# Kernel optimization log

Measured on AMD Instinct MI355X. Metric: run time of the kernel, lower is better.

Reference implementation:

```python
import jax, jax.numpy as jnp
import numpy as np

B, C, H, W = 8, 64, 256, 256
M1, M2 = 16, 16  # half of n_modes=(32,32); rfft last dim keeps n_modes[-1]//2


def setup_inputs() -> dict:
    key = jax.random.key(0)
    ks = jax.random.split(key, 7)
    scale = 1.0 / (C * C)
    return {
        "x": jax.random.normal(ks[0], (B, C, H, W), dtype=jnp.float32),
        "w1r": scale * jax.random.normal(ks[1], (C, C, M1, M2), dtype=jnp.float32),
        "w1i": scale * jax.random.normal(ks[2], (C, C, M1, M2), dtype=jnp.float32),
        "w2r": scale * jax.random.normal(ks[3], (C, C, M1, M2), dtype=jnp.float32),
        "w2i": scale * jax.random.normal(ks[4], (C, C, M1, M2), dtype=jnp.float32),
        "conv_w": jax.random.normal(ks[5], (C, C), dtype=jnp.float32) / np.sqrt(C),
        "conv_b": jax.random.normal(ks[6], (C,), dtype=jnp.float32) * 0.01,
    }


def reference(x, w1r, w1i, w2r, w2i, conv_w, conv_b):
    # ---- SpectralConv branch ----
    # rfft2 over spatial dims with 'ortho' norm: [b, c, H, W//2+1] complex
    x_ft = jnp.fft.rfftn(x, axes=(2, 3), norm="ortho")
    w1 = w1r + 1j * w1i  # positive-frequency corner weights [i, o, m1, m2]
    w2 = w2r + 1j * w2i  # negative-frequency corner weights
    top = jnp.einsum("bixy,ioxy->boxy", x_ft[:, :, :M1, :M2], w1)
    bot = jnp.einsum("bixy,ioxy->boxy", x_ft[:, :, -M1:, :M2], w2)
    out_ft = jnp.zeros((B, C, H, W // 2 + 1), dtype=x_ft.dtype)
    out_ft = out_ft.at[:, :, :M1, :M2].set(top)
    out_ft = out_ft.at[:, :, -M1:, :M2].set(bot)
    x1 = jnp.fft.irfftn(out_ft, s=(H, W), axes=(2, 3), norm="ortho")
    # ---- 1x1 Conv1d residual branch (channel mixing) ----
    x2 = jnp.einsum("oi,bixy->boxy", conv_w, x) + conv_b[None, :, None, None]
    return x1 + x2
```

## Files before the change

kernel.cpp:

```cpp
#include <hip/hip_runtime.h>
#include <math.h>


#define TWOPI_256 0.024543692606170259f
#define INV256    0.00390625f

#define NX   262144
#define NWT  2097152
#define NZ   2097152
#define O_TA  0
#define O_TB  4096
#define O_XR  20480
#define O_XI  (O_XR + NX)
#define O_WTR (O_XI + NX)
#define O_WTI (O_WTR + NWT)
#define O_YRA (O_WTI + NWT)
#define O_YIA (O_YRA + NX)
#define O_ZR  (O_YIA + NX)
#define O_ZI  (O_ZR + NZ)
#define O_TT  (O_ZI + NZ)
#define O_TD  (O_TT + 4096)
#define O_YRB (O_TD + 16384)
#define O_YIB (O_YRB + NX)

using s16x8 = __attribute__((ext_vector_type(8))) short;
using f32x4 = __attribute__((ext_vector_type(4))) float;
using u32x4 = __attribute__((ext_vector_type(4))) unsigned;

__device__ __forceinline__ unsigned short f2bf(float f) {
    union { float f; unsigned u; } a; a.f = f;
    unsigned r = (a.u + 0x7fffu + ((a.u >> 16) & 1u)) >> 16;
    return (unsigned short)r;
}

__device__ __forceinline__ unsigned bfpack(float a, float b) {
    union { float f; unsigned u; } x, y; x.f = a; y.f = b;
    return ((x.u + 0x8000u) >> 16) | ((y.u + 0x8000u) & 0xffff0000u);
}

__global__ __launch_bounds__(256) void ktabs(unsigned short* __restrict__ tA,
                                             unsigned short* __restrict__ tB,
                                             unsigned short* __restrict__ tD,
                                             unsigned short* __restrict__ tT) {
    int idx = blockIdx.x * 256 + threadIdx.x;
    if (idx < 8192) {
        int col = idx >> 8, w = idx & 255;
        int ky = col & 15;
        int mm = (ky * w) & 255;
        float s, c; sincosf((float)mm * TWOPI_256, &s, &c);
        tA[idx] = f2bf(col < 16 ? c * INV256 : -s * INV256);
    } else if (idx < 40960) {
        int j = idx - 8192;
        int kx2 = j >> 9, k = j & 511, h = k >> 1, p = k & 1;
        int kxi = kx2 & 31;
        int kx = (kxi < 16) ? kxi : (224 + kxi);
        int mm = (kx * h) & 255;
        float s, c; sincosf((float)mm * TWOPI_256, &s, &c);
        float v;
        if (kx2 < 32) v = p ? s : c;
        else          v = p ? c : -s;
        tB[j] = f2bf(v);
    } else if (idx < 73728) {
        int j = idx - 40960;
        int ri = j >> 14, rem = j & 16383;
        int h = rem >> 6, k = rem & 63, kxi = k >> 1, p = k & 1;
        int kx = (kxi < 16) ? kxi : (224 + kxi);
        int mm = (kx * h) & 255;
        float s, c; sincosf((float)mm * TWOPI_256, &s, &c);
        float v;
        if (ri == 0) v = p ? -s : c;
        else         v = p ? c : s;
        tD[j] = f2bf(v);
    } else {
        int j = idx - 73728;
        int w = j >> 5, kk = j & 31, ky = kk >> 1;
        int mm = (ky * w) & 255;
        float s, c; sincosf((float)mm * TWOPI_256, &s, &c);
        tT[j] = f2bf((kk & 1) ? -s : c);
    }
}

__global__ __launch_bounds__(256, 2) void kab_fwd(const float* __restrict__ x,
                                                  const unsigned short* __restrict__ tA,
                                                  const unsigned short* __restrict__ tB,
                                                  float* __restrict__ Xr,
                                                  float* __restrict__ Xi) {
    __shared__ __align__(16) unsigned short xt[16384];
    __shared__ __align__(16) unsigned int   ub[4096];
    const int tid  = threadIdx.x;
    const int bc   = blockIdx.x;
    const int m    = tid & 15;
    const int g    = (tid >> 4) & 3;
    const int wave = tid >> 6;

    const float* xp = x + (size_t)bc * 65536;
    const int hh = tid >> 4;
    const int w4 = tid & 15;

    f32x4 acc[2][4];
#pragma unroll
    for (int a = 0; a < 2; ++a)
#pragma unroll
        for (int fn = 0; fn < 4; ++fn)
#pragma unroll
            for (int r = 0; r < 4; ++r) acc[a][fn][r] = 0.f;

    float4 stg[2][16];
#pragma unroll
    for (int it = 0; it < 16; ++it)
        stg[0][it] = *reinterpret_cast<const float4*>(xp + (it * 16 + hh) * 256 + w4 * 4);

#pragma unroll
    for (int ch = 0; ch < 4; ++ch) {
        const int cur = ch & 1;
        if (ch < 3) {
#pragma unroll
            for (int it = 0; it < 16; ++it)
                stg[cur ^ 1][it] = *reinterpret_cast<const float4*>(
                    xp + (it * 16 + hh) * 256 + (ch + 1) * 64 + w4 * 4);
        }
#pragma unroll
        for (int it = 0; it < 16; ++it) {
            int h = it * 16 + hh;
            float4 v = stg[cur][it];
            unsigned lo = bfpack(v.x, v.y);
            unsigned hi = bfpack(v.z, v.w);
            int wl  = w4 * 4;
            int blk = (wl >> 3) ^ (h & 7);
            char* p = reinterpret_cast<char*>(xt) + (h << 7) + (blk << 4) + ((wl & 7) << 1);
            *reinterpret_cast<uint2*>(p) = make_uint2(lo, hi);
        }
        __syncthreads();
#pragma unroll
        for (int ks = 0; ks < 2; ++ks) {
            s16x8 a0 = *reinterpret_cast<const s16x8*>(tA + m * 256        + ch * 64 + ks * 32 + 8 * g);
            s16x8 a1 = *reinterpret_cast<const s16x8*>(tA + (16 + m) * 256 + ch * 64 + ks * 32 + 8 * g);
#pragma unroll
            for (int fn = 0; fn < 4; ++fn) {
                int h   = wave * 64 + fn * 16 + m;
                int blk = (4 * ks + g) ^ (h & 7);
                s16x8 bf = *reinterpret_cast<const s16x8*>(
                    reinterpret_cast<const char*>(xt) + (h << 7) + (blk << 4));
                acc[0][fn] = __builtin_amdgcn_mfma_f32_16x16x32_bf16(a0, bf, acc[0][fn], 0, 0, 0);
                acc[1][fn] = __builtin_amdgcn_mfma_f32_16x16x32_bf16(a1, bf, acc[1][fn], 0, 0, 0);
            }
        }
        __syncthreads();
    }

#pragma unroll
    for (int fn = 0; fn < 4; ++fn) {
        int h = wave * 64 + fn * 16 + m;
#pragma unroll
        for (int r = 0; r < 4; ++r) {
            int ky = 4 * g + r;
            unsigned pk = bfpack(acc[0][fn][r], acc[1][fn][r]);
            int blk = (h >> 2) ^ (ky & 7);
            ub[ky * 256 + blk * 4 + (h & 3)] = pk;
        }
    }
    __syncthreads();

    f32x4 acc2;
#pragma unroll
    for (int r = 0; r < 4; ++r) acc2[r] = 0.f;
#pragma unroll
    for (int ks = 0; ks < 16; ++ks) {
        s16x8 a2 = *reinterpret_cast<const s16x8*>(tB + (wave * 16 + m) * 512 + ks * 32 + 8 * g);
        int blk = (4 * ks + g) ^ (m & 7);
        s16x8 b2 = *reinterpret_cast<const s16x8*>(
            reinterpret_cast<const char*>(ub) + m * 1024 + (blk << 4));
        acc2 = __builtin_amdgcn_mfma_f32_16x16x32_bf16(a2, b2, acc2, 0, 0, 0);
    }
#pragma unroll
    for (int r = 0; r < 4; ++r) {
        int kx2 = wave * 16 + 4 * g + r;
        if (kx2 < 32) Xr[(size_t)bc * 512 + kx2 * 16 + m]        = acc2[r];
        else          Xi[(size_t)bc * 512 + (kx2 - 32) * 16 + m] = acc2[r];
    }
}

__global__ __launch_bounds__(256) void kw_prep(const float* __restrict__ w1r,
                                               const float* __restrict__ w1i,
                                               const float* __restrict__ w2r,
                                               const float* __restrict__ w2i,
                                               float* __restrict__ Wtr,
                                               float* __restrict__ Wti) {
    __shared__ float lds[128][65];
    const int tid = threadIdx.x;
    const int a = blockIdx.x >> 6;
    const int i = blockIdx.x & 63;
    const float* src = (a == 0) ? w1r : (a == 1) ? w1i : (a == 2) ? w2r : w2i;
    float* dst = (a & 1) ? Wti : Wtr;
    const int kxoff = (a >> 1) << 4;
    const float* sp = src + (size_t)i * 16384;

    for (int p = 0; p < 2; ++p) {
        if (p) __syncthreads();
#pragma unroll
        for (int it = 0; it < 8; ++it) {
            int f4 = it * 256 + tid;
            int o = f4 >> 5, j4 = f4 & 31;
            float4 v = *reinterpret_cast<const float4*>(sp + o * 256 + p * 128 + j4 * 4);
            lds[j4 * 4 + 0][o] = v.x; lds[j4 * 4 + 1][o] = v.y;
            lds[j4 * 4 + 2][o] = v.z; lds[j4 * 4 + 3][o] = v.w;
        }
        __syncthreads();
        const int o = tid & 63, mq = tid >> 6;
#pragma unroll
        for (int r = 0; r < 32; ++r) {
            int lm = r * 4 + mq;
            int mky = p * 128 + lm;
            int mm = mky >> 4, ky = mky & 15;
            dst[((((size_t)(kxoff + mm)) * 16 + ky) * 64 + i) * 64 + o] = lds[lm][o];
        }
    }
}

__global__ __launch_bounds__(256) void kc_mix(const float* __restrict__ Xr,
                                              const float* __restrict__ Xi,
                                              const float* __restrict__ Wtr,
                                              const float* __restrict__ Wti,
                                              float* __restrict__ YrA,
                                              float* __restrict__ YiA,
                                              float* __restrict__ YrB,
                                              float* __restrict__ YiB) {
    __shared__ float xsr[256], xsi[256];
    const int tid  = threadIdx.x;
    const int mode = blockIdx.x >> 1;
    const int ih   = blockIdx.x & 1;
    {
        int b = tid >> 5, il = tid & 31;
        xsr[tid] = Xr[(size_t)(b * 64 + ih * 32 + il) * 512 + mode];
        xsi[tid] = Xi[(size_t)(b * 64 + ih * 32 + il) * 512 + mode];
    }
    __syncthreads();
    const int o = tid & 63, bg = tid >> 6;
    float yr0 = 0.f, yi0 = 0.f, yr1 = 0.f, yi1 = 0.f;
    const float* wrp = Wtr + (size_t)mode * 4096 + ih * 2048;
    const float* wip = Wti + (size_t)mode * 4096 + ih * 2048;
#pragma unroll 8
    for (int i = 0; i < 32; ++i) {
        float wr = wrp[i * 64 + o], wi = wip[i * 64 + o];
        float xr = xsr[bg * 32 + i],        xi = xsi[bg * 32 + i];
        yr0 += xr * wr - xi * wi;  yi0 += xr * wi + xi * wr;
        float xr2 = xsr[(bg + 4) * 32 + i], xi2 = xsi[(bg + 4) * 32 + i];
        yr1 += xr2 * wr - xi2 * wi;  yi1 += xr2 * wi + xi2 * wr;
    }
    float* Yr = ih ? YrB : YrA;
    float* Yi = ih ? YiB : YiA;
    const int kxi = mode >> 4, kym = mode & 15;
    const size_t e0 = ((size_t)bg * 64 + o) * 512 + kym * 32 + kxi;
    const size_t e1 = ((size_t)(bg + 4) * 64 + o) * 512 + kym * 32 + kxi;
    Yr[e0] = yr0;  Yi[e0] = yi0;
    Yr[e1] = yr1;  Yi[e1] = yi1;
}

__global__ __launch_bounds__(256) void kd_mfma(const float* __restrict__ YrA,
                                               const float* __restrict__ YiA,
                                               const float* __restrict__ YrB,
                                               const float* __restrict__ YiB,
                                               const unsigned short* __restrict__ tD,
                                               float* __restrict__ Zr,
                                               float* __restrict__ Zi) {
    __shared__ __align__(16) unsigned short at[4096];
    __shared__ __align__(16) float zt[64][68];
    const int tid = threadIdx.x;
    const int bid = blockIdx.x;
    const int b  = bid >> 7;
    const int og = (bid >> 3) & 15;
    const int ri = (bid >> 2) & 1;
    const int hs = bid & 3;

    {
        const int row = tid >> 2, q = tid & 3;
        const int ol = row >> 4, ky = row & 15;
        const float sc = (ky == 0) ? INV256 : 2.f * INV256;
        const size_t yb = ((size_t)(b * 64 + og * 4 + ol)) * 512 + ky * 32 + q * 8;
        f32x4 r0 = *reinterpret_cast<const f32x4*>(YrA + yb)     + *reinterpret_cast<const f32x4*>(YrB + yb);
        f32x4 r1 = *reinterpret_cast<const f32x4*>(YrA + yb + 4) + *reinterpret_cast<const f32x4*>(YrB + yb + 4);
        f32x4 i0 = *reinterpret_cast<const f32x4*>(YiA + yb)     + *reinterpret_cast<const f32x4*>(YiB + yb);
        f32x4 i1 = *reinterpret_cast<const f32x4*>(YiA + yb + 4) + *reinterpret_cast<const f32x4*>(YiB + yb + 4);
        unsigned wbuf[8];
#pragma unroll
        for (int t = 0; t < 4; ++t) {
            wbuf[t]     = bfpack(r0[t] * sc, i0[t] * sc);
            wbuf[4 + t] = bfpack(r1[t] * sc, i1[t] * sc);
        }
        char* base = reinterpret_cast<char*>(at) + row * 128;
        *reinterpret_cast<uint4*>(base + (((2 * q)     ^ (row & 7)) << 4)) = *reinterpret_cast<uint4*>(&wbuf[0]);
        *reinterpret_cast<uint4*>(base + (((2 * q + 1) ^ (row & 7)) << 4)) = *reinterpret_cast<uint4*>(&wbuf[4]);
    }
    __syncthreads();

    const int m = tid & 15, g = (tid >> 4) & 3, wid = tid >> 6;
    const unsigned short* td = tD + ri * 16384;
    const int hg = hs * 64 + wid * 16 + m;

    f32x4 acc[4];
#pragma unroll
    for (int mf = 0; mf < 4; ++mf)
#pragma unroll
        for (int r = 0; r < 4; ++r) acc[mf][r] = 0.f;

#pragma unroll
    for (int ks = 0; ks < 2; ++ks) {
        s16x8 bf = *reinterpret_cast<const s16x8*>(td + hg * 64 + ks * 32 + 8 * g);
#pragma unroll
        for (int mf = 0; mf < 4; ++mf) {
            s16x8 af = *reinterpret_cast<const s16x8*>(
                reinterpret_cast<const char*>(at) + (mf * 16 + m) * 128
                + (((4 * ks + g) ^ (m & 7)) << 4));
            acc[mf] = __builtin_amdgcn_mfma_f32_16x16x32_bf16(af, bf, acc[mf], 0, 0, 0);
        }
    }

#pragma unroll
    for (int mf = 0; mf < 4; ++mf)
#pragma unroll
        for (int r = 0; r < 4; ++r)
            zt[wid * 16 + m][mf * 16 + 4 * g + r] = acc[mf][r];
    __syncthreads();

    float* Zd = ri ? Zi : Zr;
    const int ol = tid >> 6, hloc = (tid >> 2) & 15, kg = tid & 3;
#pragma unroll
    for (int hq = 0; hq < 4; ++hq) {
        f32x4 v = *reinterpret_cast<const f32x4*>(&zt[hq * 16 + hloc][ol * 16 + 4 * kg]);
        size_t off = (((size_t)(b * 64 + og * 4 + ol)) * 256 + hs * 64 + hq * 16 + hloc) * 16 + 4 * kg;
        *reinterpret_cast<f32x4*>(Zd + off) = v;
    }
}

__global__ __launch_bounds__(256) void ke_mfma(const float* __restrict__ x,
                                               const float* __restrict__ Zr,
                                               const float* __restrict__ Zi,
                                               const float* __restrict__ cw,
                                               const float* __restrict__ bias,
                                               const unsigned short* __restrict__ ttab,
                                               float* __restrict__ out) {
    __shared__ unsigned int bsx[4096];
    const int tid = threadIdx.x;
    const int b  = blockIdx.x >> 9;
    const int h  = (blockIdx.x >> 1) & 255;
    const int wh = blockIdx.x & 1;
    const int wbase = wh * 128;

    const size_t xbase = ((size_t)b * 64) * 65536 + (size_t)h * 256 + wbase;
    const int wl4 = (tid & 31) * 4;
    const int ipg = tid >> 5;
    float4 va[4], vb[4];
#pragma unroll
    for (int it = 0; it < 4; ++it) {
        int ip = it * 8 + ipg;
        va[it] = *reinterpret_cast<const float4*>(x + xbase + (size_t)(2 * ip) * 65536 + wl4);
        vb[it] = *reinterpret_cast<const float4*>(x + xbase + (size_t)(2 * ip + 1) * 65536 + wl4);
    }

    const int m = tid & 15;
    const int g = (tid >> 4) & 3;
    const int wave = tid >> 6;
    const int o = wave * 16 + m;

    s16x8 a0, a1, az;
    {
        f32x4 p  = *reinterpret_cast<const f32x4*>(cw + o * 64 + 8 * g);
        f32x4 q  = *reinterpret_cast<const f32x4*>(cw + o * 64 + 8 * g + 4);
        f32x4 p2 = *reinterpret_cast<const f32x4*>(cw + o * 64 + 32 + 8 * g);
        f32x4 q2 = *reinterpret_cast<const f32x4*>(cw + o * 64 + 32 + 8 * g + 4);
        size_t zoff = (((size_t)b * 64 + o) * 256 + h) * 16 + 4 * g;
        f32x4 zr = *reinterpret_cast<const f32x4*>(Zr + zoff);
        f32x4 zi = *reinterpret_cast<const f32x4*>(Zi + zoff);
        u32x4 t0 = {bfpack(p[0], p[1]),  bfpack(p[2], p[3]),
                    bfpack(q[0], q[1]),  bfpack(q[2], q[3])};
        u32x4 t1 = {bfpack(p2[0], p2[1]), bfpack(p2[2], p2[3]),
                    bfpack(q2[0], q2[1]), bfpack(q2[2], q2[3])};
        u32x4 tz = {bfpack(zr[0], zi[0]), bfpack(zr[1], zi[1]),
                    bfpack(zr[2], zi[2]), bfpack(zr[3], zi[3])};
        a0 = __builtin_bit_cast(s16x8, t0);
        a1 = __builtin_bit_cast(s16x8, t1);
        az = __builtin_bit_cast(s16x8, tz);
    }
    s16x8 btr[8];
#pragma unroll
    for (int f = 0; f < 8; ++f) {
        int w = wbase + f * 16 + m;
        btr[f] = *reinterpret_cast<const s16x8*>(ttab + w * 32 + 8 * g);
    }
    f32x4 bv = *reinterpret_cast<const f32x4*>(bias + wave * 16 + 4 * g);

#pragma unroll
    for (int it = 0; it < 4; ++it) {
        int ip = it * 8 + ipg;
        const float* pa = reinterpret_cast<const float*>(&va[it]);
        const float* pb = reinterpret_cast<const float*>(&vb[it]);
#pragma unroll
        for (int j = 0; j < 4; ++j) {
            int wl = wl4 + j;
            int c = (wl ^ (wl >> 3)) & 7;
            unsigned pk = bfpack(pa[j], pb[j]);
            bsx[(wl << 5) + ((((ip >> 2) ^ c) << 2) | (ip & 3))] = pk;
        }
    }
    __syncthreads();

    f32x4 acc[8];
#pragma unroll
    for (int f = 0; f < 8; ++f)
#pragma unroll
        for (int r = 0; r < 4; ++r) acc[f][r] = 0.f;

#pragma unroll
    for (int f = 0; f < 8; ++f) {
        int wl = f * 16 + m;
        int c = (wl ^ (wl >> 3)) & 7;
        const char* rb = reinterpret_cast<const char*>(bsx) + (wl << 7);
        s16x8 bx0 = *reinterpret_cast<const s16x8*>(rb + ((g ^ c) << 4));
        s16x8 bx1 = *reinterpret_cast<const s16x8*>(rb + (((4 + g) ^ c) << 4));
        acc[f] = __builtin_amdgcn_mfma_f32_16x16x32_bf16(a0, bx0, acc[f], 0, 0, 0);
        acc[f] = __builtin_amdgcn_mfma_f32_16x16x32_bf16(a1, bx1, acc[f], 0, 0, 0);
        acc[f] = __builtin_amdgcn_mfma_f32_16x16x32_bf16(az, btr[f], acc[f], 0, 0, 0);
    }

    float* ob = out + ((size_t)(b * 64 + wave * 16 + 4 * g)) * 65536 + (size_t)h * 256 + wbase;
#pragma unroll
    for (int f = 0; f < 8; ++f) {
#pragma unroll
        for (int r = 0; r < 4; ++r)
            ob[(size_t)r * 65536 + f * 16 + m] = acc[f][r] + bv[r];
    }
}

extern "C" void kernel_launch(void* const* d_in, const int* in_sizes, int n_in,
                              void* d_out, int out_size, void* d_ws, size_t ws_size,
                              hipStream_t stream) {
    const float* x   = (const float*)d_in[0];
    const float* w1r = (const float*)d_in[1];
    const float* w1i = (const float*)d_in[2];
    const float* w2r = (const float*)d_in[3];
    const float* w2i = (const float*)d_in[4];
    const float* cw  = (const float*)d_in[5];
    const float* cb  = (const float*)d_in[6];
    float* out = (float*)d_out;
    float* ws  = (float*)d_ws;
    unsigned short* tA   = (unsigned short*)(ws + O_TA);
    unsigned short* tB   = (unsigned short*)(ws + O_TB);
    unsigned short* ttab = (unsigned short*)(ws + O_TT);
    unsigned short* tD   = (unsigned short*)(ws + O_TD);

    ktabs<<<320, 256, 0, stream>>>(tA, tB, tD, ttab);
    kw_prep<<<256, 256, 0, stream>>>(w1r, w1i, w2r, w2i, ws + O_WTR, ws + O_WTI);
    kab_fwd<<<512, 256, 0, stream>>>(x, tA, tB, ws + O_XR, ws + O_XI);
    kc_mix<<<1024, 256, 0, stream>>>(ws + O_XR, ws + O_XI, ws + O_WTR, ws + O_WTI,
                                     ws + O_YRA, ws + O_YIA, ws + O_YRB, ws + O_YIB);
    kd_mfma<<<1024, 256, 0, stream>>>(ws + O_YRA, ws + O_YIA, ws + O_YRB, ws + O_YIB,
                                      tD, ws + O_ZR, ws + O_ZI);
    ke_mfma<<<4096, 256, 0, stream>>>(x, ws + O_ZR, ws + O_ZI, cw, cb, ttab, out);
}
```

Before: 127.5 us.

## Split forward DFT over H halves and store Z intermediate as bf16

The forward-transform kernel now runs two blocks per (b,c) slice, each taking half of the H rows. Each half writes a partial spectrum to its own buffer, and the mixing kernel adds the two partials when it loads them. This halves LDS and register use per block, allowing occupancy 4 and twice as many blocks. Separately, the Z intermediate is written as packed bf16 in the layout the final kernel loads directly as an MFMA operand, which halves that traffic and removes the repacking. The cost is an extra partial buffer to read and sum, and the twiddle table layout changes to match.

```diff
diff --git a/kernel.cpp b/kernel.cpp
--- a/kernel.cpp
+++ b/kernel.cpp
@@ -7,21 +7,23 @@
 
 #define NX   262144
 #define NWT  2097152
-#define NZ   2097152
-#define O_TA  0
-#define O_TB  4096
-#define O_XR  20480
-#define O_XI  (O_XR + NX)
-#define O_WTR (O_XI + NX)
-#define O_WTI (O_WTR + NWT)
-#define O_YRA (O_WTI + NWT)
-#define O_YIA (O_YRA + NX)
-#define O_ZR  (O_YIA + NX)
-#define O_ZI  (O_ZR + NZ)
-#define O_TT  (O_ZI + NZ)
-#define O_TD  (O_TT + 4096)
-#define O_YRB (O_TD + 16384)
-#define O_YIB (O_YRB + NX)
+#define NZH  1048576
+#define O_TA   0
+#define O_TB   4096
+#define O_XRA  20480
+#define O_XIA  (O_XRA + NX)
+#define O_XRB  (O_XIA + NX)
+#define O_XIB  (O_XRB + NX)
+#define O_WTR  (O_XIB + NX)
+#define O_WTI  (O_WTR + NWT)
+#define O_YRA  (O_WTI + NWT)
+#define O_YIA  (O_YRA + NX)
+#define O_YRB  (O_YIA + NX)
+#define O_YIB  (O_YRB + NX)
+#define O_ZRB  (O_YIB + NX)
+#define O_ZIB  (O_ZRB + NZH)
+#define O_TT   (O_ZIB + NZH)
+#define O_TD   (O_TT + 4096)
 
 using s16x8 = __attribute__((ext_vector_type(8))) short;
 using f32x4 = __attribute__((ext_vector_type(4))) float;
@@ -73,41 +75,45 @@
         tD[j] = f2bf(v);
     } else {
         int j = idx - 73728;
-        int w = j >> 5, kk = j & 31, ky = kk >> 1;
+        int w = j >> 5, kk = j & 31, ky = kk & 15;
         int mm = (ky * w) & 255;
         float s, c; sincosf((float)mm * TWOPI_256, &s, &c);
-        tT[j] = f2bf((kk & 1) ? -s : c);
-    }
-}
-
-__global__ __launch_bounds__(256, 2) void kab_fwd(const float* __restrict__ x,
+        tT[j] = f2bf(kk < 16 ? c : -s);
+    }
+}
+
+__global__ __launch_bounds__(256, 4) void kab_fwd(const float* __restrict__ x,
                                                   const unsigned short* __restrict__ tA,
                                                   const unsigned short* __restrict__ tB,
-                                                  float* __restrict__ Xr,
-                                                  float* __restrict__ Xi) {
-    __shared__ __align__(16) unsigned short xt[16384];
-    __shared__ __align__(16) unsigned int   ub[4096];
+                                                  float* __restrict__ XrA,
+                                                  float* __restrict__ XiA,
+                                                  float* __restrict__ XrB,
+                                                  float* __restrict__ XiB) {
+    __shared__ __align__(16) unsigned short xt[8192];
+    __shared__ __align__(16) unsigned int   ub[2048];
     const int tid  = threadIdx.x;
-    const int bc   = blockIdx.x;
+    const int bc   = blockIdx.x >> 1;
+    const int hhf  = blockIdx.x & 1;
+    const int hbase = hhf << 7;
     const int m    = tid & 15;
     const int g    = (tid >> 4) & 3;
     const int wave = tid >> 6;
 
-    const float* xp = x + (size_t)bc * 65536;
+    const float* xp = x + (size_t)bc * 65536 + (size_t)hbase * 256;
     const int hh = tid >> 4;
     const int w4 = tid & 15;
 
-    f32x4 acc[2][4];
+    f32x4 acc[2][2];
 #pragma unroll
     for (int a = 0; a < 2; ++a)
 #pragma unroll
-        for (int fn = 0; fn < 4; ++fn)
+        for (int fn = 0; fn < 2; ++fn)
 #pragma unroll
             for (int r = 0; r < 4; ++r) acc[a][fn][r] = 0.f;
 
-    float4 stg[2][16];
-#pragma unroll
-    for (int it = 0; it < 16; ++it)
+    float4 stg[2][8];
+#pragma unroll
+    for (int it = 0; it < 8; ++it)
         stg[0][it] = *reinterpret_cast<const float4*>(xp + (it * 16 + hh) * 256 + w4 * 4);
 
 #pragma unroll
@@ -115,12 +121,12 @@
         const int cur = ch & 1;
         if (ch < 3) {
 #pragma unroll
-            for (int it = 0; it < 16; ++it)
+            for (int it = 0; it < 8; ++it)
                 stg[cur ^ 1][it] = *reinterpret_cast<const float4*>(
                     xp + (it * 16 + hh) * 256 + (ch + 1) * 64 + w4 * 4);
         }
 #pragma unroll
-        for (int it = 0; it < 16; ++it) {
+        for (int it = 0; it < 8; ++it) {
             int h = it * 16 + hh;
             float4 v = stg[cur][it];
             unsigned lo = bfpack(v.x, v.y);
@@ -136,8 +142,8 @@
             s16x8 a0 = *reinterpret_cast<const s16x8*>(tA + m * 256        + ch * 64 + ks * 32 + 8 * g);
             s16x8 a1 = *reinterpret_cast<const s16x8*>(tA + (16 + m) * 256 + ch * 64 + ks * 32 + 8 * g);
 #pragma unroll
-            for (int fn = 0; fn < 4; ++fn) {
-                int h   = wave * 64 + fn * 16 + m;
+            for (int fn = 0; fn < 2; ++fn) {
+                int h   = wave * 32 + fn * 16 + m;
                 int blk = (4 * ks + g) ^ (h & 7);
                 s16x8 bf = *reinterpret_cast<const s16x8*>(
                     reinterpret_cast<const char*>(xt) + (h << 7) + (blk << 4));
@@ -149,14 +155,14 @@
     }
 
 #pragma unroll
-    for (int fn = 0; fn < 4; ++fn) {
-        int h = wave * 64 + fn * 16 + m;
+    for (int fn = 0; fn < 2; ++fn) {
+        int h = wave * 32 + fn * 16 + m;
 #pragma unroll
         for (int r = 0; r < 4; ++r) {
             int ky = 4 * g + r;
             unsigned pk = bfpack(acc[0][fn][r], acc[1][fn][r]);
             int blk = (h >> 2) ^ (ky & 7);
-            ub[ky * 256 + blk * 4 + (h & 3)] = pk;
+            ub[ky * 128 + blk * 4 + (h & 3)] = pk;
         }
     }
     __syncthreads();
@@ -165,13 +171,15 @@
 #pragma unroll
     for (int r = 0; r < 4; ++r) acc2[r] = 0.f;
 #pragma unroll
-    for (int ks = 0; ks < 16; ++ks) {
-        s16x8 a2 = *reinterpret_cast<const s16x8*>(tB + (wave * 16 + m) * 512 + ks * 32 + 8 * g);
+    for (int ks = 0; ks < 8; ++ks) {
+        s16x8 a2 = *reinterpret_cast<const s16x8*>(tB + (wave * 16 + m) * 512 + hbase * 2 + ks * 32 + 8 * g);
         int blk = (4 * ks + g) ^ (m & 7);
         s16x8 b2 = *reinterpret_cast<const s16x8*>(
-            reinterpret_cast<const char*>(ub) + m * 1024 + (blk << 4));
+            reinterpret_cast<const char*>(ub) + m * 512 + (blk << 4));
         acc2 = __builtin_amdgcn_mfma_f32_16x16x32_bf16(a2, b2, acc2, 0, 0, 0);
     }
+    float* Xr = hhf ? XrB : XrA;
+    float* Xi = hhf ? XiB : XiA;
 #pragma unroll
     for (int r = 0; r < 4; ++r) {
         int kx2 = wave * 16 + 4 * g + r;
@@ -217,8 +225,10 @@
     }
 }
 
-__global__ __launch_bounds__(256) void kc_mix(const float* __restrict__ Xr,
-                                              const float* __restrict__ Xi,
+__global__ __launch_bounds__(256) void kc_mix(const float* __restrict__ XrA,
+                                              const float* __restrict__ XiA,
+                                              const float* __restrict__ XrB,
+                                              const float* __restrict__ XiB,
                                               const float* __restrict__ Wtr,
                                               const float* __restrict__ Wti,
                                               float* __restrict__ YrA,
@@ -231,8 +241,9 @@
     const int ih   = blockIdx.x & 1;
     {
         int b = tid >> 5, il = tid & 31;
-        xsr[tid] = Xr[(size_t)(b * 64 + ih * 32 + il) * 512 + mode];
-        xsi[tid] = Xi[(size_t)(b * 64 + ih * 32 + il) * 512 + mode];
+        size_t ofs = (size_t)(b * 64 + ih * 32 + il) * 512 + mode;
+        xsr[tid] = XrA[ofs] + XrB[ofs];
+        xsi[tid] = XiA[ofs] + XiB[ofs];
     }
     __syncthreads();
     const int o = tid & 63, bg = tid >> 6;
@@ -261,8 +272,8 @@
                                                const float* __restrict__ YrB,
                                                const float* __restrict__ YiB,
                                                const unsigned short* __restrict__ tD,
-                                               float* __restrict__ Zr,
-                                               float* __restrict__ Zi) {
+                                               unsigned short* __restrict__ Zrb,
+                                               unsigned short* __restrict__ Zib) {
     __shared__ __align__(16) unsigned short at[4096];
     __shared__ __align__(16) float zt[64][68];
     const int tid = threadIdx.x;
@@ -322,19 +333,21 @@
             zt[wid * 16 + m][mf * 16 + 4 * g + r] = acc[mf][r];
     __syncthreads();
 
-    float* Zd = ri ? Zi : Zr;
+    unsigned short* Zd = ri ? Zib : Zrb;
     const int ol = tid >> 6, hloc = (tid >> 2) & 15, kg = tid & 3;
 #pragma unroll
     for (int hq = 0; hq < 4; ++hq) {
         f32x4 v = *reinterpret_cast<const f32x4*>(&zt[hq * 16 + hloc][ol * 16 + 4 * kg]);
+        unsigned lo = bfpack(v[0], v[1]);
+        unsigned hi = bfpack(v[2], v[3]);
         size_t off = (((size_t)(b * 64 + og * 4 + ol)) * 256 + hs * 64 + hq * 16 + hloc) * 16 + 4 * kg;
-        *reinterpret_cast<f32x4*>(Zd + off) = v;
+        *reinterpret_cast<uint2*>(Zd + off) = make_uint2(lo, hi);
     }
 }
 
 __global__ __launch_bounds__(256) void ke_mfma(const float* __restrict__ x,
-                                               const float* __restrict__ Zr,
-                                               const float* __restrict__ Zi,
+                                               const unsigned short* __restrict__ Zrb,
+                                               const unsigned short* __restrict__ Zib,
                                                const float* __restrict__ cw,
                                                const float* __restrict__ bias,
                                                const unsigned short* __restrict__ ttab,
@@ -368,18 +381,15 @@
         f32x4 q  = *reinterpret_cast<const f32x4*>(cw + o * 64 + 8 * g + 4);
         f32x4 p2 = *reinterpret_cast<const f32x4*>(cw + o * 64 + 32 + 8 * g);
         f32x4 q2 = *reinterpret_cast<const f32x4*>(cw + o * 64 + 32 + 8 * g + 4);
-        size_t zoff = (((size_t)b * 64 + o) * 256 + h) * 16 + 4 * g;
-        f32x4 zr = *reinterpret_cast<const f32x4*>(Zr + zoff);
-        f32x4 zi = *reinterpret_cast<const f32x4*>(Zi + zoff);
         u32x4 t0 = {bfpack(p[0], p[1]),  bfpack(p[2], p[3]),
                     bfpack(q[0], q[1]),  bfpack(q[2], q[3])};
         u32x4 t1 = {bfpack(p2[0], p2[1]), bfpack(p2[2], p2[3]),
                     bfpack(q2[0], q2[1]), bfpack(q2[2], q2[3])};
-        u32x4 tz = {bfpack(zr[0], zi[0]), bfpack(zr[1], zi[1]),
-                    bfpack(zr[2], zi[2]), bfpack(zr[3], zi[3])};
         a0 = __builtin_bit_cast(s16x8, t0);
         a1 = __builtin_bit_cast(s16x8, t1);
-        az = __builtin_bit_cast(s16x8, tz);
+        const unsigned short* zsrc = (g < 2) ? Zrb : Zib;
+        az = *reinterpret_cast<const s16x8*>(
+            zsrc + (((size_t)b * 64 + o) * 256 + h) * 16 + (g & 1) * 8);
     }
     s16x8 btr[8];
 #pragma unroll
@@ -447,13 +457,17 @@
     unsigned short* tB   = (unsigned short*)(ws + O_TB);
     unsigned short* ttab = (unsigned short*)(ws + O_TT);
     unsigned short* tD   = (unsigned short*)(ws + O_TD);
+    unsigned short* Zrb  = (unsigned short*)(ws + O_ZRB);
+    unsigned short* Zib  = (unsigned short*)(ws + O_ZIB);
 
     ktabs<<<320, 256, 0, stream>>>(tA, tB, tD, ttab);
     kw_prep<<<256, 256, 0, stream>>>(w1r, w1i, w2r, w2i, ws + O_WTR, ws + O_WTI);
-    kab_fwd<<<512, 256, 0, stream>>>(x, tA, tB, ws + O_XR, ws + O_XI);
-    kc_mix<<<1024, 256, 0, stream>>>(ws + O_XR, ws + O_XI, ws + O_WTR, ws + O_WTI,
+    kab_fwd<<<1024, 256, 0, stream>>>(x, tA, tB, ws + O_XRA, ws + O_XIA,
+                                      ws + O_XRB, ws + O_XIB);
+    kc_mix<<<1024, 256, 0, stream>>>(ws + O_XRA, ws + O_XIA, ws + O_XRB, ws + O_XIB,
+                                     ws + O_WTR, ws + O_WTI,
                                      ws + O_YRA, ws + O_YIA, ws + O_YRB, ws + O_YIB);
     kd_mfma<<<1024, 256, 0, stream>>>(ws + O_YRA, ws + O_YIA, ws + O_YRB, ws + O_YIB,
-                                      tD, ws + O_ZR, ws + O_ZI);
-    ke_mfma<<<4096, 256, 0, stream>>>(x, ws + O_ZR, ws + O_ZI, cw, cb, ttab, out);
-}
+                                      tD, Zrb, Zib);
+    ke_mfma<<<4096, 256, 0, stream>>>(x, Zrb, Zib, cw, cb, ttab, out);
+}
```

After: 128.7 us. No clear change (+0.9%).
